# Optimization experiments

Hardware: AMD Instinct MI355X
Metric: run time of the kernel (lower is better)

Reference implementation:

```python
import jax, jax.numpy as jnp
import numpy as np

B, S, H, E, A = 64, 1024, 1024, 1024, 1024

def setup_inputs() -> dict:
    key = jax.random.key(0)
    k1, k2, k3, k4, k5 = jax.random.split(key, 5)
    return {
        "decoder_state": jax.random.normal(k1, (B, H), dtype=jnp.float32),
        "encoder_outputs": jax.random.normal(k2, (B, S, E), dtype=jnp.float32),
        "src_mask": jnp.ones((B, S), dtype=bool),
        "W_a": jax.random.normal(k3, (H, A), dtype=jnp.float32) / np.sqrt(H),
        "U_a": jax.random.normal(k4, (E, A), dtype=jnp.float32) / np.sqrt(E),
        "v_a": jax.random.normal(k5, (A,), dtype=jnp.float32) / np.sqrt(A),
    }

def reference(decoder_state, encoder_outputs, src_mask, W_a, U_a, v_a):
    # k_dec: [B, 1, A], k_enc: [B, S, A]
    k_dec = jnp.einsum('bh,ha->ba', decoder_state, W_a)[:, None, :]
    k_enc = jnp.einsum('bse,ea->bsa', encoder_outputs, U_a)
    att_hidden = jnp.tanh(k_dec + k_enc)
    scores = jnp.einsum('bsa,a->bs', att_hidden, v_a)
    scores = scores + (~src_mask).astype(scores.dtype) * (-1e9)
    weights = jax.nn.softmax(scores, axis=-1)
    ctx = jnp.einsum('bs,bse->be', weights, encoder_outputs)
    return (ctx, weights)
```

## Files before the change

### kernel.cpp

```cpp
#include <hip/hip_runtime.h>
#include <hip/hip_bf16.h>
#include <math.h>

#define NB 64
#define NS 1024
#define NH 1024
#define NE 1024
#define NA 1024

#define A_TILE 8192
#define B_TILE 16384
#define BUF_BYTES 49152
#define NT 128

typedef __attribute__((ext_vector_type(8))) short bf16x8;
typedef __attribute__((ext_vector_type(8))) unsigned short ushort8_t;
typedef __attribute__((ext_vector_type(4))) float f32x4;

__device__ __forceinline__ unsigned short f2bf(float x) {
    __hip_bfloat16 h = __float2bfloat16(x);
    return *reinterpret_cast<unsigned short*>(&h);
}
__device__ __forceinline__ float bf2f(unsigned short u) {
    __hip_bfloat16 h = *reinterpret_cast<__hip_bfloat16*>(&u);
    return __bfloat162float(h);
}
__device__ __forceinline__ float tanh_fast(float x) {
    float ax = fabsf(x);
    float e = __expf(-2.f * ax);
    float r = (1.f - e) / (1.f + e);
    return x < 0.f ? -r : r;
}
__device__ __forceinline__ int swz32(int row, int bcol) {
    return row * 64 + (bcol ^ (((row >> 1) & 3) << 4));
}
__device__ __forceinline__ void gload_lds16(const void* g, void* l) {
    __builtin_amdgcn_global_load_lds(
        (const __attribute__((address_space(1))) unsigned int*)g,
        (__attribute__((address_space(3))) unsigned int*)l, 16, 0, 0);
}

__global__ __launch_bounds__(256) void split_enc_kernel(
    const float* __restrict__ enc,
    unsigned short* __restrict__ encHiT, unsigned short* __restrict__ encLoT)
{
    const int sblk = blockIdx.x;
    const int b    = blockIdx.y;
    const int t    = threadIdx.x;
    const float* src = enc + ((size_t)b * NS + sblk * 128) * NE;
    char* hiB = (char*)encHiT + (size_t)(b * 8 + sblk) * 32 * A_TILE;
    char* loB = (char*)encLoT + (size_t)(b * 8 + sblk) * 32 * A_TILE;
    const int et   = t >> 3;
    const int bcol = (t & 7) * 8;
    for (int row = 0; row < 128; ++row) {
        const float4 v = *reinterpret_cast<const float4*>(src + (size_t)row * NE + t * 4);
        ushort4 h, l;
        h.x = f2bf(v.x); l.x = f2bf(v.x - bf2f(h.x));
        h.y = f2bf(v.y); l.y = f2bf(v.y - bf2f(h.y));
        h.z = f2bf(v.z); l.z = f2bf(v.z - bf2f(h.z));
        h.w = f2bf(v.w); l.w = f2bf(v.w - bf2f(h.w));
        const int off = (size_t)et * A_TILE + swz32(row, bcol);
        *reinterpret_cast<ushort4*>(hiB + off) = h;
        *reinterpret_cast<ushort4*>(loB + off) = l;
    }
}

__global__ __launch_bounds__(256) void split_uat_kernel(
    const float* __restrict__ Ua,
    unsigned short* __restrict__ uatHiT, unsigned short* __restrict__ uatLoT)
{
    __shared__ float ls[32][257];
    const int ac = blockIdx.x;
    const int eb = blockIdx.y;
    const int t  = threadIdx.x;
    const int a0 = ac * 256, e0 = eb * 32;
#pragma unroll
    for (int p = 0; p < 8; ++p) {
        const int flat = p * 256 + t;
        const int e = flat >> 6, q = flat & 63;
        *reinterpret_cast<float4*>(&ls[e][q * 4]) =
            *reinterpret_cast<const float4*>(Ua + (size_t)(e0 + e) * NA + a0 + q * 4);
    }
    __syncthreads();
    char* hiT = (char*)uatHiT + (size_t)(ac * 32 + eb) * B_TILE;
    char* loT = (char*)uatLoT + (size_t)(ac * 32 + eb) * B_TILE;
#pragma unroll
    for (int p = 0; p < 4; ++p) {
        const int flat = p * 256 + t;
        const int a = flat >> 2, o = flat & 3;
        ushort8_t h8, l8;
#pragma unroll
        for (int j = 0; j < 8; ++j) {
            const float x = ls[o * 8 + j][a];
            const unsigned short hh = f2bf(x);
            h8[j] = hh;
            l8[j] = f2bf(x - bf2f(hh));
        }
        const int off = swz32(a, o * 16);
        *reinterpret_cast<int4*>(hiT + off) = *reinterpret_cast<int4*>(&h8);
        *reinterpret_cast<int4*>(loT + off) = *reinterpret_cast<int4*>(&l8);
    }
}

__global__ __launch_bounds__(256) void kdec_kernel(
    const float* __restrict__ dec, const float* __restrict__ Wa,
    float* __restrict__ kdec)
{
    __shared__ float dls[NH];
    const int b = blockIdx.x;
    const int a = blockIdx.y * 256 + threadIdx.x;
    for (int i = threadIdx.x; i < NH; i += 256) dls[i] = dec[b * NH + i];
    __syncthreads();
    float acc = 0.f;
#pragma unroll 8
    for (int h = 0; h < NH; ++h) acc += dls[h] * Wa[(size_t)h * NA + a];
    kdec[b * NA + a] = acc;
}

__global__ __launch_bounds__(512, 2) void scores_mfma2_kernel(
    const unsigned short* __restrict__ encHiT, const unsigned short* __restrict__ encLoT,
    const unsigned short* __restrict__ uatHiT, const unsigned short* __restrict__ uatLoT,
    const float* __restrict__ kdec, const float* __restrict__ va,
    float* __restrict__ scores)
{
    __shared__ __align__(16) char lds[3 * BUF_BYTES];
    __shared__ float scLds[4][128];

    const int t    = threadIdx.x;
    const int sblk = blockIdx.x;
    const int b    = blockIdx.y;
    const int lane = t & 63;
    const int wid  = t >> 6;
    const int wr   = wid >> 2;
    const int wc   = wid & 3;
    const int lrow = lane & 15;
    const int kb   = (lane >> 4) * 16;

    const char* aHiB = (const char*)encHiT + (size_t)(b * 8 + sblk) * 32 * A_TILE;
    const char* aLoB = (const char*)encLoT + (size_t)(b * 8 + sblk) * 32 * A_TILE;
    const char* bHiB = (const char*)uatHiT;
    const char* bLoB = (const char*)uatLoT;

    int aOff[4], bOff[4];
#pragma unroll
    for (int f = 0; f < 4; ++f) {
        aOff[f] = swz32(wr * 64 + f * 16 + lrow, kb);
        bOff[f] = swz32(wc * 64 + f * 16 + lrow, kb);
    }

    float kd[4][4], vv[4][4];
#pragma unroll
    for (int ac = 0; ac < 4; ++ac)
#pragma unroll
        for (int fj = 0; fj < 4; ++fj) {
            const int a = ac * 256 + wc * 64 + fj * 16 + lrow;
            kd[ac][fj] = kdec[(size_t)b * NA + a];
            vv[ac][fj] = va[a];
        }

    auto STAGE = [&](int g, int buf) {
        const int ac2 = g >> 5, et2 = g & 31;
        const char* aHi = aHiB + (size_t)et2 * A_TILE;
        const char* aLo = aLoB + (size_t)et2 * A_TILE;
        const char* bHi = bHiB + (size_t)(ac2 * 32 + et2) * B_TILE;
        const char* bLo = bLoB + (size_t)(ac2 * 32 + et2) * B_TILE;
        char* dst = lds + buf * BUF_BYTES;
        const int so = t * 16;
        const int wo = wid * 1024;
        gload_lds16(aHi + so,        dst + 0 * 8192 + wo);
        gload_lds16(aLo + so,        dst + 1 * 8192 + wo);
        gload_lds16(bHi + so,        dst + 2 * 8192 + wo);
        gload_lds16(bHi + 8192 + so, dst + 3 * 8192 + wo);
        gload_lds16(bLo + so,        dst + 4 * 8192 + wo);
        gload_lds16(bLo + 8192 + so, dst + 5 * 8192 + wo);
    };

    float scp[4][4];
#pragma unroll
    for (int i = 0; i < 4; ++i)
#pragma unroll
        for (int r = 0; r < 4; ++r) scp[i][r] = 0.f;

    STAGE(0, 0);
    STAGE(1, 1);

    int cur = 0;
#pragma unroll
    for (int ac = 0; ac < 4; ++ac) {
        f32x4 acc[4][4];
#pragma unroll
        for (int fi = 0; fi < 4; ++fi)
#pragma unroll
            for (int fj = 0; fj < 4; ++fj) acc[fi][fj] = (f32x4){0.f, 0.f, 0.f, 0.f};

        for (int et = 0; et < 32; ++et) {
            const int g = ac * 32 + et;
            if (g + 2 < NT) {
                int nb = cur + 2; if (nb >= 3) nb -= 3;
                STAGE(g + 2, nb);
                asm volatile("s_waitcnt vmcnt(12)" ::: "memory");
            } else if (g + 1 < NT) {
                asm volatile("s_waitcnt vmcnt(6)" ::: "memory");
            } else {
                asm volatile("s_waitcnt vmcnt(0)" ::: "memory");
            }
            asm volatile("s_barrier" ::: "memory");

            const char* L = lds + cur * BUF_BYTES;
            bf16x8 aH[4], aL[4], bH[4], bL[4];
#pragma unroll
            for (int f = 0; f < 4; ++f) {
                aH[f] = *reinterpret_cast<const bf16x8*>(L + aOff[f]);
                aL[f] = *reinterpret_cast<const bf16x8*>(L + A_TILE + aOff[f]);
                bH[f] = *reinterpret_cast<const bf16x8*>(L + 2 * A_TILE + bOff[f]);
                bL[f] = *reinterpret_cast<const bf16x8*>(L + 2 * A_TILE + B_TILE + bOff[f]);
            }
            __builtin_amdgcn_s_setprio(1);
#pragma unroll
            for (int fi = 0; fi < 4; ++fi)
#pragma unroll
                for (int fj = 0; fj < 4; ++fj) {
                    acc[fi][fj] = __builtin_amdgcn_mfma_f32_16x16x32_bf16(aH[fi], bH[fj], acc[fi][fj], 0, 0, 0);
                    acc[fi][fj] = __builtin_amdgcn_mfma_f32_16x16x32_bf16(aH[fi], bL[fj], acc[fi][fj], 0, 0, 0);
                    acc[fi][fj] = __builtin_amdgcn_mfma_f32_16x16x32_bf16(aL[fi], bH[fj], acc[fi][fj], 0, 0, 0);
                }
            __builtin_amdgcn_s_setprio(0);
            __builtin_amdgcn_sched_barrier(0);
            asm volatile("s_waitcnt lgkmcnt(0)" ::: "memory");
            asm volatile("s_barrier" ::: "memory");
            cur += 1; if (cur >= 3) cur -= 3;
        }

#pragma unroll
        for (int fj = 0; fj < 4; ++fj)
#pragma unroll
            for (int fi = 0; fi < 4; ++fi)
#pragma unroll
                for (int r = 0; r < 4; ++r)
                    scp[fi][r] += tanh_fast(kd[ac][fj] + acc[fi][fj][r]) * vv[ac][fj];
    }

#pragma unroll
    for (int fi = 0; fi < 4; ++fi)
#pragma unroll
        for (int r = 0; r < 4; ++r) {
            float v = scp[fi][r];
            v += __shfl_xor(v, 1);
            v += __shfl_xor(v, 2);
            v += __shfl_xor(v, 4);
            v += __shfl_xor(v, 8);
            if (lrow == 0)
                scLds[wc][wr * 64 + fi * 16 + (lane >> 4) * 4 + r] = v;
        }
    __syncthreads();
    if (t < 128)
        scores[(size_t)b * NS + sblk * 128 + t] =
            scLds[0][t] + scLds[1][t] + scLds[2][t] + scLds[3][t];
}

__global__ __launch_bounds__(256) void softmax_kernel(
    const float* __restrict__ scores, const int* __restrict__ mask,
    float* __restrict__ out)
{
    __shared__ float red[8];
    const int b = blockIdx.x;
    const int t = threadIdx.x;
    float v[4];
    float mx = -INFINITY;
#pragma unroll
    for (int i = 0; i < 4; ++i) {
        const int s = t + i * 256;
        float x = scores[b * NS + s];
        if (mask[b * NS + s] == 0) x += -1e9f;
        v[i] = x;
        mx = fmaxf(mx, x);
    }
    for (int off = 1; off < 64; off <<= 1) mx = fmaxf(mx, __shfl_xor(mx, off));
    const int wid = t >> 6;
    if ((t & 63) == 0) red[wid] = mx;
    __syncthreads();
    mx = fmaxf(fmaxf(red[0], red[1]), fmaxf(red[2], red[3]));
    float sum = 0.f;
#pragma unroll
    for (int i = 0; i < 4; ++i) { v[i] = expf(v[i] - mx); sum += v[i]; }
    for (int off = 1; off < 64; off <<= 1) sum += __shfl_xor(sum, off);
    if ((t & 63) == 0) red[4 + wid] = sum;
    __syncthreads();
    sum = red[4] + red[5] + red[6] + red[7];
    const float inv = 1.f / sum;
#pragma unroll
    for (int i = 0; i < 4; ++i) {
        const int s = t + i * 256;
        out[NB * NE + b * NS + s] = v[i] * inv;
        out[b * NE + s] = 0.f;
    }
}

__global__ __launch_bounds__(256) void ctx_kernel(
    const float* __restrict__ enc, const float* __restrict__ w,
    float* __restrict__ ctx)
{
    __shared__ float wls[128];
    const int b  = blockIdx.x;
    const int ec = blockIdx.y;
    const int ss = blockIdx.z;
    const int t  = threadIdx.x;
    if (t < 128) wls[t] = w[b * NS + ss * 128 + t];
    __syncthreads();
    const int e = ec * 256 + t;
    const float* p = enc + ((size_t)b * NS + ss * 128) * NE + e;
    float acc = 0.f;
#pragma unroll 4
    for (int s = 0; s < 128; ++s) acc += wls[s] * p[(size_t)s * NE];
    atomicAdd(&ctx[b * NE + e], acc);
}

extern "C" void kernel_launch(void* const* d_in, const int* in_sizes, int n_in,
                              void* d_out, int out_size, void* d_ws, size_t ws_size,
                              hipStream_t stream)
{
    const float* dec  = (const float*)d_in[0];
    const float* enc  = (const float*)d_in[1];
    const int*   mask = (const int*)d_in[2];
    const float* Wa   = (const float*)d_in[3];
    const float* Ua   = (const float*)d_in[4];
    const float* va   = (const float*)d_in[5];
    float* out = (float*)d_out;

    float* kdec   = (float*)d_ws;
    float* scores = kdec + NB * NA;
    unsigned short* uatHiT = (unsigned short*)(scores + NB * NS);
    unsigned short* uatLoT = uatHiT + (size_t)NA * NE;
    unsigned short* encHiT = uatLoT + (size_t)NA * NE;
    unsigned short* encLoT = encHiT + (size_t)NB * NS * NE;

    kdec_kernel<<<dim3(NB, NA / 256), 256, 0, stream>>>(dec, Wa, kdec);
    split_uat_kernel<<<dim3(4, 32), 256, 0, stream>>>(Ua, uatHiT, uatLoT);
    split_enc_kernel<<<dim3(8, NB), 256, 0, stream>>>(enc, encHiT, encLoT);
    scores_mfma2_kernel<<<dim3(8, NB), 512, 0, stream>>>(
        encHiT, encLoT, uatHiT, uatLoT, kdec, va, scores);
    softmax_kernel<<<dim3(NB), 256, 0, stream>>>(scores, mask, out);
    ctx_kernel<<<dim3(NB, NE / 256, NS / 128), 256, 0, stream>>>(enc, out + NB * NE, out);
}
```

Measured before the change: 1.097 ms.

## Interleave half-stage prefetches with per-column MFMA phases and widen split stores

The main scores kernel now splits each K-step into four phases, one per B fragment column. B fragments are loaded just in time, and the prefetch of tile g+2 is split into two halves issued between phases, so global-to-LDS traffic overlaps with MFMA work. Barriers between phases keep the waves in lockstep, in the style of ping-pong scheduling. The enc split kernel is also restructured to write 16-byte swizzled chunks per thread instead of 8-byte ones, to improve store efficiency. The cost is many more barriers per iteration and finer-grained vmcnt bookkeeping, which could serialise the waves.

New measurement: 1.149 ms. 1.05x slower.

```diff
diff --git a/kernel.cpp b/kernel.cpp
--- a/kernel.cpp
+++ b/kernel.cpp
@@ -50,18 +50,28 @@
     const float* src = enc + ((size_t)b * NS + sblk * 128) * NE;
     char* hiB = (char*)encHiT + (size_t)(b * 8 + sblk) * 32 * A_TILE;
     char* loB = (char*)encLoT + (size_t)(b * 8 + sblk) * 32 * A_TILE;
-    const int et   = t >> 3;
-    const int bcol = (t & 7) * 8;
-    for (int row = 0; row < 128; ++row) {
-        const float4 v = *reinterpret_cast<const float4*>(src + (size_t)row * NE + t * 4);
-        ushort4 h, l;
-        h.x = f2bf(v.x); l.x = f2bf(v.x - bf2f(h.x));
-        h.y = f2bf(v.y); l.y = f2bf(v.y - bf2f(h.y));
-        h.z = f2bf(v.z); l.z = f2bf(v.z - bf2f(h.z));
-        h.w = f2bf(v.w); l.w = f2bf(v.w - bf2f(h.w));
-        const int off = (size_t)et * A_TILE + swz32(row, bcol);
-        *reinterpret_cast<ushort4*>(hiB + off) = h;
-        *reinterpret_cast<ushort4*>(loB + off) = l;
+    for (int et = 0; et < 32; ++et) {
+#pragma unroll
+        for (int i = 0; i < 2; ++i) {
+            const int flat = i * 256 + t;
+            const int row  = flat >> 2;
+            const int c16  = (flat & 3) * 16;
+            const int ecol = et * 32 + c16 / 2;
+            const float4 v0 = *reinterpret_cast<const float4*>(src + (size_t)row * NE + ecol);
+            const float4 v1 = *reinterpret_cast<const float4*>(src + (size_t)row * NE + ecol + 4);
+            ushort8_t h, l;
+            h[0] = f2bf(v0.x); l[0] = f2bf(v0.x - bf2f(h[0]));
+            h[1] = f2bf(v0.y); l[1] = f2bf(v0.y - bf2f(h[1]));
+            h[2] = f2bf(v0.z); l[2] = f2bf(v0.z - bf2f(h[2]));
+            h[3] = f2bf(v0.w); l[3] = f2bf(v0.w - bf2f(h[3]));
+            h[4] = f2bf(v1.x); l[4] = f2bf(v1.x - bf2f(h[4]));
+            h[5] = f2bf(v1.y); l[5] = f2bf(v1.y - bf2f(h[5]));
+            h[6] = f2bf(v1.z); l[6] = f2bf(v1.z - bf2f(h[6]));
+            h[7] = f2bf(v1.w); l[7] = f2bf(v1.w - bf2f(h[7]));
+            const int off = et * A_TILE + swz32(row, c16);
+            *reinterpret_cast<int4*>(hiB + off) = *reinterpret_cast<int4*>(&h);
+            *reinterpret_cast<int4*>(loB + off) = *reinterpret_cast<int4*>(&l);
+        }
     }
 }
 
@@ -117,7 +127,7 @@
     kdec[b * NA + a] = acc;
 }
 
-__global__ __launch_bounds__(512, 2) void scores_mfma2_kernel(
+__global__ __launch_bounds__(512, 2) void scores_mfma3_kernel(
     const unsigned short* __restrict__ encHiT, const unsigned short* __restrict__ encLoT,
     const unsigned short* __restrict__ uatHiT, const unsigned short* __restrict__ uatLoT,
     const float* __restrict__ kdec, const float* __restrict__ va,
@@ -157,8 +167,9 @@
             kd[ac][fj] = kdec[(size_t)b * NA + a];
             vv[ac][fj] = va[a];
         }
-
-    auto STAGE = [&](int g, int buf) {
+    asm volatile("s_waitcnt vmcnt(0)" ::: "memory");
+
+    auto STAGE_HALF = [&](int g, int buf, int half) {
         const int ac2 = g >> 5, et2 = g & 31;
         const char* aHi = aHiB + (size_t)et2 * A_TILE;
         const char* aLo = aLoB + (size_t)et2 * A_TILE;
@@ -167,12 +178,15 @@
         char* dst = lds + buf * BUF_BYTES;
         const int so = t * 16;
         const int wo = wid * 1024;
-        gload_lds16(aHi + so,        dst + 0 * 8192 + wo);
-        gload_lds16(aLo + so,        dst + 1 * 8192 + wo);
-        gload_lds16(bHi + so,        dst + 2 * 8192 + wo);
-        gload_lds16(bHi + 8192 + so, dst + 3 * 8192 + wo);
-        gload_lds16(bLo + so,        dst + 4 * 8192 + wo);
-        gload_lds16(bLo + 8192 + so, dst + 5 * 8192 + wo);
+        if (half == 0) {
+            gload_lds16(aHi + so,        dst + 0 * 8192 + wo);
+            gload_lds16(aLo + so,        dst + 1 * 8192 + wo);
+            gload_lds16(bHi + so,        dst + 2 * 8192 + wo);
+        } else {
+            gload_lds16(bHi + 8192 + so, dst + 3 * 8192 + wo);
+            gload_lds16(bLo + so,        dst + 4 * 8192 + wo);
+            gload_lds16(bLo + 8192 + so, dst + 5 * 8192 + wo);
+        }
     };
 
     float scp[4][4];
@@ -181,8 +195,10 @@
 #pragma unroll
         for (int r = 0; r < 4; ++r) scp[i][r] = 0.f;
 
-    STAGE(0, 0);
-    STAGE(1, 1);
+    STAGE_HALF(0, 0, 0); STAGE_HALF(0, 0, 1);
+    STAGE_HALF(1, 1, 0); STAGE_HALF(1, 1, 1);
+    asm volatile("s_waitcnt vmcnt(6)" ::: "memory");
+    asm volatile("s_barrier" ::: "memory");
 
     int cur = 0;
 #pragma unroll
@@ -195,39 +211,91 @@
 
         for (int et = 0; et < 32; ++et) {
             const int g = ac * 32 + et;
-            if (g + 2 < NT) {
-                int nb = cur + 2; if (nb >= 3) nb -= 3;
-                STAGE(g + 2, nb);
-                asm volatile("s_waitcnt vmcnt(12)" ::: "memory");
-            } else if (g + 1 < NT) {
-                asm volatile("s_waitcnt vmcnt(6)" ::: "memory");
-            } else {
-                asm volatile("s_waitcnt vmcnt(0)" ::: "memory");
-            }
-            asm volatile("s_barrier" ::: "memory");
-
             const char* L = lds + cur * BUF_BYTES;
-            bf16x8 aH[4], aL[4], bH[4], bL[4];
+            const bool st = (g + 2 < NT);
+            int nb = cur + 2; if (nb >= 3) nb -= 3;
+
+            bf16x8 aH[4], aL[4];
 #pragma unroll
             for (int f = 0; f < 4; ++f) {
                 aH[f] = *reinterpret_cast<const bf16x8*>(L + aOff[f]);
                 aL[f] = *reinterpret_cast<const bf16x8*>(L + A_TILE + aOff[f]);
-                bH[f] = *reinterpret_cast<const bf16x8*>(L + 2 * A_TILE + bOff[f]);
-                bL[f] = *reinterpret_cast<const bf16x8*>(L + 2 * A_TILE + B_TILE + bOff[f]);
             }
-            __builtin_amdgcn_s_setprio(1);
-#pragma unroll
-            for (int fi = 0; fi < 4; ++fi)
-#pragma unroll
-                for (int fj = 0; fj < 4; ++fj) {
-                    acc[fi][fj] = __builtin_amdgcn_mfma_f32_16x16x32_bf16(aH[fi], bH[fj], acc[fi][fj], 0, 0, 0);
-                    acc[fi][fj] = __builtin_amdgcn_mfma_f32_16x16x32_bf16(aH[fi], bL[fj], acc[fi][fj], 0, 0, 0);
-                    acc[fi][fj] = __builtin_amdgcn_mfma_f32_16x16x32_bf16(aL[fi], bH[fj], acc[fi][fj], 0, 0, 0);
+            {
+                bf16x8 bh = *reinterpret_cast<const bf16x8*>(L + 2 * A_TILE + bOff[0]);
+                bf16x8 bl = *reinterpret_cast<const bf16x8*>(L + 2 * A_TILE + B_TILE + bOff[0]);
+                asm volatile("s_barrier" ::: "memory");
+                asm volatile("s_waitcnt lgkmcnt(0)" ::: "memory");
+                __builtin_amdgcn_sched_barrier(0);
+                __builtin_amdgcn_s_setprio(1);
+#pragma unroll
+                for (int fi = 0; fi < 4; ++fi) {
+                    acc[fi][0] = __builtin_amdgcn_mfma_f32_16x16x32_bf16(aH[fi], bh, acc[fi][0], 0, 0, 0);
+                    acc[fi][0] = __builtin_amdgcn_mfma_f32_16x16x32_bf16(aH[fi], bl, acc[fi][0], 0, 0, 0);
+                    acc[fi][0] = __builtin_amdgcn_mfma_f32_16x16x32_bf16(aL[fi], bh, acc[fi][0], 0, 0, 0);
                 }
-            __builtin_amdgcn_s_setprio(0);
-            __builtin_amdgcn_sched_barrier(0);
-            asm volatile("s_waitcnt lgkmcnt(0)" ::: "memory");
-            asm volatile("s_barrier" ::: "memory");
+                __builtin_amdgcn_s_setprio(0);
+                __builtin_amdgcn_sched_barrier(0);
+                asm volatile("s_barrier" ::: "memory");
+            }
+            {
+                bf16x8 bh = *reinterpret_cast<const bf16x8*>(L + 2 * A_TILE + bOff[1]);
+                bf16x8 bl = *reinterpret_cast<const bf16x8*>(L + 2 * A_TILE + B_TILE + bOff[1]);
+                if (st) STAGE_HALF(g + 2, nb, 0);
+                asm volatile("s_barrier" ::: "memory");
+                asm volatile("s_waitcnt lgkmcnt(0)" ::: "memory");
+                __builtin_amdgcn_sched_barrier(0);
+                __builtin_amdgcn_s_setprio(1);
+#pragma unroll
+                for (int fi = 0; fi < 4; ++fi) {
+                    acc[fi][1] = __builtin_amdgcn_mfma_f32_16x16x32_bf16(aH[fi], bh, acc[fi][1], 0, 0, 0);
+                    acc[fi][1] = __builtin_amdgcn_mfma_f32_16x16x32_bf16(aH[fi], bl, acc[fi][1], 0, 0, 0);
+                    acc[fi][1] = __builtin_amdgcn_mfma_f32_16x16x32_bf16(aL[fi], bh, acc[fi][1], 0, 0, 0);
+                }
+                __builtin_amdgcn_s_setprio(0);
+                __builtin_amdgcn_sched_barrier(0);
+                asm volatile("s_barrier" ::: "memory");
+            }
+            {
+                bf16x8 bh = *reinterpret_cast<const bf16x8*>(L + 2 * A_TILE + bOff[2]);
+                bf16x8 bl = *reinterpret_cast<const bf16x8*>(L + 2 * A_TILE + B_TILE + bOff[2]);
+                if (st) STAGE_HALF(g + 2, nb, 1);
+                asm volatile("s_barrier" ::: "memory");
+                asm volatile("s_waitcnt lgkmcnt(0)" ::: "memory");
+                __builtin_amdgcn_sched_barrier(0);
+                __builtin_amdgcn_s_setprio(1);
+#pragma unroll
+                for (int fi = 0; fi < 4; ++fi) {
+                    acc[fi][2] = __builtin_amdgcn_mfma_f32_16x16x32_bf16(aH[fi], bh, acc[fi][2], 0, 0, 0);
+                    acc[fi][2] = __builtin_amdgcn_mfma_f32_16x16x32_bf16(aH[fi], bl, acc[fi][2], 0, 0, 0);
+                    acc[fi][2] = __builtin_amdgcn_mfma_f32_16x16x32_bf16(aL[fi], bh, acc[fi][2], 0, 0, 0);
+                }
+                __builtin_amdgcn_s_setprio(0);
+                __builtin_amdgcn_sched_barrier(0);
+                asm volatile("s_barrier" ::: "memory");
+            }
+            {
+                bf16x8 bh = *reinterpret_cast<const bf16x8*>(L + 2 * A_TILE + bOff[3]);
+                bf16x8 bl = *reinterpret_cast<const bf16x8*>(L + 2 * A_TILE + B_TILE + bOff[3]);
+                if (st) {
+                    asm volatile("s_waitcnt vmcnt(6)" ::: "memory");
+                } else if (g + 1 < NT) {
+                    asm volatile("s_waitcnt vmcnt(0)" ::: "memory");
+                }
+                asm volatile("s_barrier" ::: "memory");
+                asm volatile("s_waitcnt lgkmcnt(0)" ::: "memory");
+                __builtin_amdgcn_sched_barrier(0);
+                __builtin_amdgcn_s_setprio(1);
+#pragma unroll
+                for (int fi = 0; fi < 4; ++fi) {
+                    acc[fi][3] = __builtin_amdgcn_mfma_f32_16x16x32_bf16(aH[fi], bh, acc[fi][3], 0, 0, 0);
+                    acc[fi][3] = __builtin_amdgcn_mfma_f32_16x16x32_bf16(aH[fi], bl, acc[fi][3], 0, 0, 0);
+                    acc[fi][3] = __builtin_amdgcn_mfma_f32_16x16x32_bf16(aL[fi], bh, acc[fi][3], 0, 0, 0);
+                }
+                __builtin_amdgcn_s_setprio(0);
+                __builtin_amdgcn_sched_barrier(0);
+                asm volatile("s_barrier" ::: "memory");
+            }
             cur += 1; if (cur >= 3) cur -= 3;
         }
 
@@ -337,7 +405,7 @@
     kdec_kernel<<<dim3(NB, NA / 256), 256, 0, stream>>>(dec, Wa, kdec);
     split_uat_kernel<<<dim3(4, 32), 256, 0, stream>>>(Ua, uatHiT, uatLoT);
     split_enc_kernel<<<dim3(8, NB), 256, 0, stream>>>(enc, encHiT, encLoT);
-    scores_mfma2_kernel<<<dim3(8, NB), 512, 0, stream>>>(
+    scores_mfma3_kernel<<<dim3(8, NB), 512, 0, stream>>>(
         encHiT, encLoT, uatHiT, uatLoT, kdec, va, scores);
     softmax_kernel<<<dim3(NB), 256, 0, stream>>>(scores, mask, out);
     ctx_kernel<<<dim3(NB, NE / 256, NS / 128), 256, 0, stream>>>(enc, out + NB * NE, out);
```
